# Performance work log

Measured on AMD Instinct MI355X. Metric: run time of the kernel, lower is better.

The kernel has to match this reference:

```python
import jax, jax.numpy as jnp
import numpy as np

B, T, C, H = 4, 8192, 1024, 8
D = C // H  # head dim = 128

def setup_inputs() -> dict:
    key = jax.random.key(0)
    ks = jax.random.split(key, 9)
    s = 1.0 / np.sqrt(C)
    return {
        "x":  jax.random.normal(ks[0], (B, T, C), dtype=jnp.float32),
        "Wq": jax.random.normal(ks[1], (C, C), dtype=jnp.float32) * s,
        "bq": jax.random.normal(ks[2], (C,), dtype=jnp.float32) * s,
        "Wk": jax.random.normal(ks[3], (C, C), dtype=jnp.float32) * s,
        "bk": jax.random.normal(ks[4], (C,), dtype=jnp.float32) * s,
        "Wv": jax.random.normal(ks[5], (C, C), dtype=jnp.float32) * s,
        "bv": jax.random.normal(ks[6], (C,), dtype=jnp.float32) * s,
        "Wp": jax.random.normal(ks[7], (C, C), dtype=jnp.float32) * s,
        "bp": jax.random.normal(ks[8], (C,), dtype=jnp.float32) * s,
    }

def _heads(t):
    # [B, T, C] -> [B, H, T, D]
    return t.reshape(B, T, H, D).transpose(0, 2, 1, 3)

def reference(x, Wq, bq, Wk, bk, Wv, bv, Wp, bp):
    q = _heads(x @ Wq + bq)  # [B,H,T,D]
    k = _heads(x @ Wk + bk)
    v = _heads(x @ Wv + bv)
    # attn_type == 'l1': softmax over head/feature dim
    q = jax.nn.softmax(q, axis=-1)
    k = jax.nn.softmax(k, axis=-1)
    k_sum = k.sum(axis=-2, keepdims=True)                      # [B,H,1,D]
    D_inv = 1.0 / (q * k_sum).sum(axis=-1, keepdims=True)      # [B,H,T,1]
    context = jnp.einsum('bhtd,bhte->bhde', k, v)              # [B,H,D,D]
    y = jnp.einsum('bhtd,bhde->bhte', q, context) * D_inv + q  # [B,H,T,D]
    y = y.transpose(0, 2, 1, 3).reshape(B, T, C)               # merge heads
    return y @ Wp + bp
```

## Files before the change

kernel.cpp:

```cpp
#include <hip/hip_runtime.h>

#define B_ 4
#define T_ 8192
#define C_ 1024
#define H_ 8
#define D_ 128
#define M_ (B_*T_)
#define NKC_ 32

typedef __attribute__((ext_vector_type(8))) short bf16x8;
typedef __attribute__((ext_vector_type(4))) float f32x4;

__device__ __forceinline__ unsigned short f2b(float f) {
  union { float f; unsigned int u; } x; x.f = f;
  unsigned int r = x.u + 0x7fffu + ((x.u >> 16) & 1u);
  return (unsigned short)(r >> 16);
}
__device__ __forceinline__ float b2f(unsigned short u) {
  union { float f; unsigned int u; } x; x.u = ((unsigned int)u) << 16; return x.f;
}

__device__ __forceinline__ void gl2lds16(const void* g, void* l) {
  __builtin_amdgcn_global_load_lds((const __attribute__((address_space(1))) void*)g,
                                   (__attribute__((address_space(3))) void*)l, 16, 0, 0);
}

__device__ __forceinline__ int swz_id() {
  const int orig = blockIdx.y * 8 + blockIdx.x;
  return (orig & 7) * 256 + (orig >> 3);
}

template<typename OutT, bool VTRANS=false>
__global__ __launch_bounds__(256) void mfma_gemm_bias(
    const unsigned short* __restrict__ A,
    const unsigned short* __restrict__ Bt,
    const float* __restrict__ bias,
    OutT* __restrict__ out,
    int M, int N, int K)
{
  __shared__ __align__(16) char lds[32768];
  char* As = lds;
  char* Bs = lds + 16384;
  const int tid  = threadIdx.x;
  const int w    = tid >> 6, lane = tid & 63;
  const int id   = swz_id();
  const int bm   = (id >> 3) * 128, bn = (id & 7) * 128;
  const int wrow = (w >> 1) * 64, wcol = (w & 1) * 64;
  const int l15  = lane & 15, l4 = lane >> 4;

  f32x4 acc[4][4] = {};

  const int srow = lane >> 3;
  const int sc   = lane & 7;

  for (int k0 = 0; k0 < K; k0 += 64) {
    __syncthreads();
#pragma unroll
    for (int j = 0; j < 4; ++j) {
      const int ch  = w * 4 + j;
      const int row = ch * 8 + srow;
      const int kc  = sc ^ (row & 7);
      const char* ga = (const char*)(A  + (size_t)(bm + row) * K + k0) + kc * 16;
      const char* gb = (const char*)(Bt + (size_t)(bn + row) * K + k0) + kc * 16;
      gl2lds16(ga, As + ch * 1024 + lane * 16);
      gl2lds16(gb, Bs + ch * 1024 + lane * 16);
    }
    __syncthreads();

#pragma unroll
    for (int ks = 0; ks < 2; ++ks) {
      bf16x8 af[4], bf[4];
#pragma unroll
      for (int i = 0; i < 4; ++i) {
        const int m  = wrow + i * 16 + l15;
        const int n  = wcol + i * 16 + l15;
        const int kc = ks * 4 + l4;
        af[i] = *(const bf16x8*)(As + m * 128 + ((kc ^ (m & 7)) * 16));
        bf[i] = *(const bf16x8*)(Bs + n * 128 + ((kc ^ (n & 7)) * 16));
      }
#pragma unroll
      for (int i = 0; i < 4; ++i)
#pragma unroll
        for (int j = 0; j < 4; ++j)
          acc[i][j] = __builtin_amdgcn_mfma_f32_16x16x32_bf16(af[i], bf[j], acc[i][j], 0, 0, 0);
    }
  }

#pragma unroll
  for (int j = 0; j < 4; ++j) {
    const int col = bn + wcol + j * 16 + l15;
    const float bv = bias[col];
    if constexpr (VTRANS) {
      const int e = wcol + j * 16 + l15;
      const int h = bn >> 7;
#pragma unroll
      for (int i = 0; i < 4; ++i) {
        const int m = bm + wrow + i * 16 + l4 * 4;
        const int b = m >> 13, t = m & 8191;
        union { unsigned short u[4]; uint2 v; } pk;
#pragma unroll
        for (int r = 0; r < 4; ++r) pk.u[r] = f2b(acc[i][j][r] + bv);
        *(uint2*)((unsigned short*)out + ((size_t)(b * H_ + h) * D_ + e) * T_ + t) = pk.v;
      }
    } else {
#pragma unroll
      for (int i = 0; i < 4; ++i) {
        const int rbase = bm + wrow + i * 16 + l4 * 4;
#pragma unroll
        for (int r = 0; r < 4; ++r) {
          const float val = acc[i][j][r] + bv;
          if constexpr (sizeof(OutT) == 4)
            out[(size_t)(rbase + r) * N + col] = val;
          else
            ((unsigned short*)out)[(size_t)(rbase + r) * N + col] = f2b(val);
        }
      }
    }
  }
}

template<bool KMODE>
__global__ __launch_bounds__(256) void qk_gemm_softmax(
    const unsigned short* __restrict__ A,
    const unsigned short* __restrict__ Bt,
    const float* __restrict__ bias,
    unsigned short* __restrict__ kT,
    unsigned short* __restrict__ qb,
    float* __restrict__ ksum,
    const float* __restrict__ ksum_in,
    float* __restrict__ dinv)
{
  __shared__ __align__(16) char lds[32768];
  char* As = lds;
  char* Bs = lds + 16384;
  const int tid  = threadIdx.x;
  const int w    = tid >> 6, lane = tid & 63;
  const int id   = swz_id();
  const int bm   = (id >> 3) * 128, bn = (id & 7) * 128;
  const int wrow = w * 32;
  const int l15  = lane & 15, l4 = lane >> 4;

  f32x4 acc[2][8] = {};
  const int srow = lane >> 3;
  const int sc   = lane & 7;

  for (int k0 = 0; k0 < 1024; k0 += 64) {
    __syncthreads();
#pragma unroll
    for (int j = 0; j < 4; ++j) {
      const int ch  = w * 4 + j;
      const int row = ch * 8 + srow;
      const int kc  = sc ^ (row & 7);
      gl2lds16((const char*)(A  + (size_t)(bm + row) * 1024 + k0) + kc * 16, As + ch * 1024 + lane * 16);
      gl2lds16((const char*)(Bt + (size_t)(bn + row) * 1024 + k0) + kc * 16, Bs + ch * 1024 + lane * 16);
    }
    __syncthreads();

#pragma unroll
    for (int ks = 0; ks < 2; ++ks) {
      bf16x8 af[2], bf[8];
      const int kc = ks * 4 + l4;
#pragma unroll
      for (int i = 0; i < 2; ++i) {
        const int m = wrow + i * 16 + l15;
        af[i] = *(const bf16x8*)(As + m * 128 + ((kc ^ (m & 7)) * 16));
      }
#pragma unroll
      for (int j = 0; j < 8; ++j) {
        const int n = j * 16 + l15;
        bf[j] = *(const bf16x8*)(Bs + n * 128 + ((kc ^ (n & 7)) * 16));
      }
#pragma unroll
      for (int i = 0; i < 2; ++i)
#pragma unroll
        for (int j = 0; j < 8; ++j)
          acc[i][j] = __builtin_amdgcn_mfma_f32_16x16x32_bf16(af[i], bf[j], acc[i][j], 0, 0, 0);
    }
  }

  float bvj[8];
#pragma unroll
  for (int j = 0; j < 8; ++j) bvj[j] = bias[bn + j * 16 + l15];

#pragma unroll
  for (int i = 0; i < 2; ++i)
#pragma unroll
    for (int r = 0; r < 4; ++r) {
      float v[8];
      float mx = -1e30f;
#pragma unroll
      for (int j = 0; j < 8; ++j) { v[j] = acc[i][j][r] + bvj[j]; mx = fmaxf(mx, v[j]); }
#pragma unroll
      for (int off = 8; off > 0; off >>= 1) mx = fmaxf(mx, __shfl_xor(mx, off, 64));
      float s = 0.f;
#pragma unroll
      for (int j = 0; j < 8; ++j) { v[j] = expf(v[j] - mx); s += v[j]; }
#pragma unroll
      for (int off = 8; off > 0; off >>= 1) s += __shfl_xor(s, off, 64);
      const float inv = 1.0f / s;
#pragma unroll
      for (int j = 0; j < 8; ++j) acc[i][j][r] = v[j] * inv;
    }

  const int h  = bn >> 7;
  const int b  = bm >> 13;
  const int bh = b * 8 + h;

  if constexpr (KMODE) {
    float csum[8];
#pragma unroll
    for (int j = 0; j < 8; ++j) csum[j] = 0.f;
#pragma unroll
    for (int j = 0; j < 8; ++j) {
      const int d = j * 16 + l15;
#pragma unroll
      for (int i = 0; i < 2; ++i) {
        const int t = (bm + wrow + i * 16 + l4 * 4) & 8191;
        union { unsigned short u[4]; uint2 v2; } pk;
#pragma unroll
        for (int r = 0; r < 4; ++r) {
          const unsigned short us = f2b(acc[i][j][r]);
          pk.u[r] = us;
          csum[j] += b2f(us);
        }
        *(uint2*)(kT + ((size_t)bh * 128 + d) * 8192 + t) = pk.v2;
      }
    }
#pragma unroll
    for (int j = 0; j < 8; ++j) {
      csum[j] += __shfl_xor(csum[j], 16, 64);
      csum[j] += __shfl_xor(csum[j], 32, 64);
    }
    __syncthreads();
    float* red = (float*)lds;
    if (l4 == 0) {
#pragma unroll
      for (int j = 0; j < 8; ++j) red[w * 128 + j * 16 + l15] = csum[j];
    }
    __syncthreads();
    if (tid < 128) {
      const float s2 = red[tid] + red[128 + tid] + red[256 + tid] + red[384 + tid];
      atomicAdd(&ksum[(size_t)bh * 128 + tid], s2);
    }
  } else {
    float ks8[8];
#pragma unroll
    for (int j = 0; j < 8; ++j) ks8[j] = ksum_in[(size_t)bh * 128 + j * 16 + l15];
#pragma unroll
    for (int i = 0; i < 2; ++i)
#pragma unroll
      for (int r = 0; r < 4; ++r) {
        const int m = bm + wrow + i * 16 + l4 * 4 + r;
        float dot = 0.f;
#pragma unroll
        for (int j = 0; j < 8; ++j) {
          acc[i][j][r] = b2f(f2b(acc[i][j][r]));
          dot += acc[i][j][r] * ks8[j];
        }
#pragma unroll
        for (int off = 8; off > 0; off >>= 1) dot += __shfl_xor(dot, off, 64);
        if (l15 == 0) dinv[(size_t)bh * 8192 + (m & 8191)] = 1.0f / dot;
#pragma unroll
        for (int j = 0; j < 8; ++j)
          qb[(size_t)m * 1024 + bn + j * 16 + l15] = f2b(acc[i][j][r]);
      }
  }
}

__global__ __launch_bounds__(256) void ctx_part_mfma(
    const unsigned short* __restrict__ kT,
    const unsigned short* __restrict__ vT,
    float* __restrict__ part)
{
  __shared__ __align__(16) char lds[32768];
  char* As = lds;
  char* Bs = lds + 16384;
  const int tid  = threadIdx.x;
  const int w    = tid >> 6, lane = tid & 63;
  const int bh   = blockIdx.y;
  const int kbase = blockIdx.x * (T_ / NKC_);
  const int wrow = (w >> 1) * 64, wcol = (w & 1) * 64;
  const int l15  = lane & 15, l4 = lane >> 4;
  const unsigned short* A  = kT + (size_t)bh * (D_ * T_);
  const unsigned short* Bt = vT + (size_t)bh * (D_ * T_);

  f32x4 acc[4][4] = {};
  const int srow = lane >> 3;
  const int sc   = lane & 7;

  for (int k0 = kbase; k0 < kbase + (T_ / NKC_); k0 += 64) {
    __syncthreads();
#pragma unroll
    for (int j = 0; j < 4; ++j) {
      const int ch  = w * 4 + j;
      const int row = ch * 8 + srow;
      const int kc  = sc ^ (row & 7);
      gl2lds16((const char*)(A  + (size_t)row * T_ + k0) + kc * 16, As + ch * 1024 + lane * 16);
      gl2lds16((const char*)(Bt + (size_t)row * T_ + k0) + kc * 16, Bs + ch * 1024 + lane * 16);
    }
    __syncthreads();

#pragma unroll
    for (int ks = 0; ks < 2; ++ks) {
      bf16x8 af[4], bf[4];
#pragma unroll
      for (int i = 0; i < 4; ++i) {
        const int m  = wrow + i * 16 + l15;
        const int n  = wcol + i * 16 + l15;
        const int kc = ks * 4 + l4;
        af[i] = *(const bf16x8*)(As + m * 128 + ((kc ^ (m & 7)) * 16));
        bf[i] = *(const bf16x8*)(Bs + n * 128 + ((kc ^ (n & 7)) * 16));
      }
#pragma unroll
      for (int i = 0; i < 4; ++i)
#pragma unroll
        for (int j = 0; j < 4; ++j)
          acc[i][j] = __builtin_amdgcn_mfma_f32_16x16x32_bf16(af[i], bf[j], acc[i][j], 0, 0, 0);
    }
  }

  float* cb = part + ((size_t)blockIdx.x * 32 + bh) * (D_ * D_);
#pragma unroll
  for (int j = 0; j < 4; ++j) {
    const int e = wcol + j * 16 + l15;
#pragma unroll
    for (int i = 0; i < 4; ++i) {
      const int dbase = wrow + i * 16 + l4 * 4;
      *(f32x4*)&cb[(size_t)e * D_ + dbase] = acc[i][j];
    }
  }
}

__global__ __launch_bounds__(256) void ctx_reduce(
    const float* __restrict__ part, unsigned short* __restrict__ ctxTb)
{
  const size_t i = ((size_t)blockIdx.x * 256 + threadIdx.x) * 4;
  float4 a = {0.f, 0.f, 0.f, 0.f};
#pragma unroll 4
  for (int p = 0; p < NKC_; ++p) {
    float4 v = *(const float4*)(part + (size_t)p * (32 * D_ * D_) + i);
    a.x += v.x; a.y += v.y; a.z += v.z; a.w += v.w;
  }
  union { unsigned short u[4]; uint2 v2; } pk;
  pk.u[0] = f2b(a.x); pk.u[1] = f2b(a.y); pk.u[2] = f2b(a.z); pk.u[3] = f2b(a.w);
  *(uint2*)(ctxTb + i) = pk.v2;
}

__global__ __launch_bounds__(256) void y_mfma(
    const unsigned short* __restrict__ qb,
    const unsigned short* __restrict__ ctxTb,
    const float* __restrict__ dinv,
    unsigned short* __restrict__ yb)
{
  __shared__ __align__(16) char lds[32768];
  char* As = lds;
  char* Bs = lds + 16384;
  const int tid  = threadIdx.x;
  const int w    = tid >> 6, lane = tid & 63;
  const int id   = swz_id();
  const int bm   = (id >> 3) * 128, bn = (id & 7) * 128;
  const int wrow = (w >> 1) * 64, wcol = (w & 1) * 64;
  const int l15  = lane & 15, l4 = lane >> 4;
  const int h = bn >> 7, b = bm >> 13, bh = b * 8 + h;
  const unsigned short* Bt = ctxTb + (size_t)bh * (D_ * D_);

  f32x4 acc[4][4] = {};
  const int srow = lane >> 3;
  const int sc   = lane & 7;

#pragma unroll
  for (int k0 = 0; k0 < 128; k0 += 64) {
    __syncthreads();
#pragma unroll
    for (int j = 0; j < 4; ++j) {
      const int ch  = w * 4 + j;
      const int row = ch * 8 + srow;
      const int kc  = sc ^ (row & 7);
      gl2lds16((const char*)(qb + (size_t)(bm + row) * 1024 + bn + k0) + kc * 16, As + ch * 1024 + lane * 16);
      gl2lds16((const char*)(Bt + (size_t)row * 128 + k0) + kc * 16, Bs + ch * 1024 + lane * 16);
    }
    __syncthreads();

#pragma unroll
    for (int ks = 0; ks < 2; ++ks) {
      bf16x8 af[4], bf[4];
#pragma unroll
      for (int i = 0; i < 4; ++i) {
        const int m  = wrow + i * 16 + l15;
        const int n  = wcol + i * 16 + l15;
        const int kc = ks * 4 + l4;
        af[i] = *(const bf16x8*)(As + m * 128 + ((kc ^ (m & 7)) * 16));
        bf[i] = *(const bf16x8*)(Bs + n * 128 + ((kc ^ (n & 7)) * 16));
      }
#pragma unroll
      for (int i = 0; i < 4; ++i)
#pragma unroll
        for (int j = 0; j < 4; ++j)
          acc[i][j] = __builtin_amdgcn_mfma_f32_16x16x32_bf16(af[i], bf[j], acc[i][j], 0, 0, 0);
    }
  }

  float di[4][4];
#pragma unroll
  for (int i = 0; i < 4; ++i)
#pragma unroll
    for (int r = 0; r < 4; ++r)
      di[i][r] = dinv[(size_t)bh * 8192 + ((bm + wrow + i * 16 + l4 * 4 + r) & 8191)];

#pragma unroll
  for (int j = 0; j < 4; ++j) {
    const int col = bn + wcol + j * 16 + l15;
#pragma unroll
    for (int i = 0; i < 4; ++i) {
      const int m = bm + wrow + i * 16 + l4 * 4;
#pragma unroll
      for (int r = 0; r < 4; ++r) {
        const float qv = b2f(qb[(size_t)(m + r) * 1024 + col]);
        yb[(size_t)(m + r) * 1024 + col] = f2b(fmaf(acc[i][j][r], di[i][r], qv));
      }
    }
  }
}

__global__ __launch_bounds__(256) void conv_bf16(
    const float* __restrict__ in, unsigned short* __restrict__ out)
{
  const size_t i = ((size_t)blockIdx.x * 256 + threadIdx.x) * 8;
  float4 a = *(const float4*)(in + i);
  float4 b = *(const float4*)(in + i + 4);
  union { unsigned short s[8]; uint4 v; } pk;
  pk.s[0] = f2b(a.x); pk.s[1] = f2b(a.y); pk.s[2] = f2b(a.z); pk.s[3] = f2b(a.w);
  pk.s[4] = f2b(b.x); pk.s[5] = f2b(b.y); pk.s[6] = f2b(b.z); pk.s[7] = f2b(b.w);
  *(uint4*)(out + i) = pk.v;
}

__global__ __launch_bounds__(256) void convT_w(
    const float* __restrict__ W, unsigned short* __restrict__ Wt)
{
  __shared__ float s[32][33];
  const int k0 = blockIdx.x * 32, n0 = blockIdx.y * 32;
  const int tx = threadIdx.x & 31, ty = threadIdx.x >> 5;
#pragma unroll
  for (int r = ty; r < 32; r += 8) s[r][tx] = W[(size_t)(k0 + r) * 1024 + n0 + tx];
  __syncthreads();
#pragma unroll
  for (int r = ty; r < 32; r += 8) Wt[(size_t)(n0 + r) * 1024 + k0 + tx] = f2b(s[tx][r]);
}

extern "C" void kernel_launch(void* const* d_in, const int* in_sizes, int n_in,
                              void* d_out, int out_size, void* d_ws, size_t ws_size,
                              hipStream_t stream)
{
  const float* x  = (const float*)d_in[0];
  const float* Wq = (const float*)d_in[1];
  const float* bq = (const float*)d_in[2];
  const float* Wk = (const float*)d_in[3];
  const float* bk = (const float*)d_in[4];
  const float* Wv = (const float*)d_in[5];
  const float* bv = (const float*)d_in[6];
  const float* Wp = (const float*)d_in[7];
  const float* bp = (const float*)d_in[8];
  float* out = (float*)d_out;

  char* w = (char*)d_ws;
  unsigned short* xb  = (unsigned short*)w;
  unsigned short* qb  = (unsigned short*)(w + (64UL  << 20));
  unsigned short* kT  = (unsigned short*)(w + (128UL << 20));
  unsigned short* vT  = (unsigned short*)(w + (192UL << 20));
  unsigned short* Wtq = (unsigned short*)(w + (256UL << 20));
  unsigned short* Wtk = Wtq + 1024*1024;
  unsigned short* Wtv = Wtk + 1024*1024;
  unsigned short* Wtp = Wtv + 1024*1024;
  float* ksum  = (float*)(w + (264UL << 20));
  float* dinv  = (float*)(w + (265UL << 20));
  unsigned short* ctxTb = (unsigned short*)(w + (266UL << 20));
  float* part  = (float*)(w + (268UL << 20));
  unsigned short* yb = xb;

  hipMemsetAsync(ksum, 0, 16384, stream);

  dim3 blk(256);
  dim3 gconvT(32, 32);
  dim3 ggemm(C_/128, M_/128);

  conv_bf16<<<dim3(M_*C_/2048), blk, 0, stream>>>(x, xb);
  convT_w<<<gconvT, blk, 0, stream>>>(Wq, Wtq);
  convT_w<<<gconvT, blk, 0, stream>>>(Wk, Wtk);
  convT_w<<<gconvT, blk, 0, stream>>>(Wv, Wtv);
  convT_w<<<gconvT, blk, 0, stream>>>(Wp, Wtp);

  qk_gemm_softmax<true><<<ggemm, blk, 0, stream>>>(xb, Wtk, bk, kT, nullptr, ksum, nullptr, nullptr);
  mfma_gemm_bias<unsigned short, true><<<ggemm, blk, 0, stream>>>(xb, Wtv, bv, vT, M_, C_, C_);
  qk_gemm_softmax<false><<<ggemm, blk, 0, stream>>>(xb, Wtq, bq, nullptr, qb, nullptr, ksum, dinv);

  ctx_part_mfma<<<dim3(NKC_, B_*H_), blk, 0, stream>>>(kT, vT, part);
  ctx_reduce   <<<dim3(32*D_*D_/1024), blk, 0, stream>>>(part, ctxTb);
  y_mfma<<<ggemm, blk, 0, stream>>>(qb, ctxTb, dinv, yb);

  mfma_gemm_bias<float><<<ggemm, blk, 0, stream>>>(yb, Wtp, bp, out, M_, C_, C_);
}
```

Measured before the change: 767.4 us.

## Double-buffer LDS staging in all MFMA GEMM kernels and merge weight transposes

Each MFMA GEMM kernel (projection GEMM, qk softmax GEMM, context partial, y GEMM) now keeps two LDS buffers. It issues the global-to-LDS loads for the next K tile before computing on the current one, with one barrier per iteration instead of two. The aim is to hide global load latency behind MFMA work. The cost is doubling LDS per block to 64KB, which may lower occupancy. The four weight transpose launches are also merged into one launch with a z grid dimension.

Result: faster. 708.5 us (-7.7%).

```diff
diff --git a/kernel.cpp b/kernel.cpp
--- a/kernel.cpp
+++ b/kernel.cpp
@@ -38,35 +38,36 @@
     OutT* __restrict__ out,
     int M, int N, int K)
 {
-  __shared__ __align__(16) char lds[32768];
-  char* As = lds;
-  char* Bs = lds + 16384;
+  __shared__ __align__(16) char lds[65536];
   const int tid  = threadIdx.x;
   const int w    = tid >> 6, lane = tid & 63;
   const int id   = swz_id();
   const int bm   = (id >> 3) * 128, bn = (id & 7) * 128;
   const int wrow = (w >> 1) * 64, wcol = (w & 1) * 64;
   const int l15  = lane & 15, l4 = lane >> 4;
-
-  f32x4 acc[4][4] = {};
-
-  const int srow = lane >> 3;
-  const int sc   = lane & 7;
-
-  for (int k0 = 0; k0 < K; k0 += 64) {
-    __syncthreads();
+  const int srow = lane >> 3, sc = lane & 7;
+
+  auto stage = [&](int buf, int k0) {
+    char* As = lds + buf * 32768;
+    char* Bs = As + 16384;
 #pragma unroll
     for (int j = 0; j < 4; ++j) {
       const int ch  = w * 4 + j;
       const int row = ch * 8 + srow;
       const int kc  = sc ^ (row & 7);
-      const char* ga = (const char*)(A  + (size_t)(bm + row) * K + k0) + kc * 16;
-      const char* gb = (const char*)(Bt + (size_t)(bn + row) * K + k0) + kc * 16;
-      gl2lds16(ga, As + ch * 1024 + lane * 16);
-      gl2lds16(gb, Bs + ch * 1024 + lane * 16);
-    }
-    __syncthreads();
-
+      gl2lds16((const char*)(A  + (size_t)(bm + row) * K + k0) + kc * 16, As + ch * 1024 + lane * 16);
+      gl2lds16((const char*)(Bt + (size_t)(bn + row) * K + k0) + kc * 16, Bs + ch * 1024 + lane * 16);
+    }
+  };
+
+  f32x4 acc[4][4] = {};
+  stage(0, 0);
+  __syncthreads();
+  int cur = 0;
+  for (int k0 = 0; k0 < K; k0 += 64) {
+    if (k0 + 64 < K) stage(cur ^ 1, k0 + 64);
+    const char* As = lds + cur * 32768;
+    const char* Bs = As + 16384;
 #pragma unroll
     for (int ks = 0; ks < 2; ++ks) {
       bf16x8 af[4], bf[4];
@@ -84,6 +85,8 @@
         for (int j = 0; j < 4; ++j)
           acc[i][j] = __builtin_amdgcn_mfma_f32_16x16x32_bf16(af[i], bf[j], acc[i][j], 0, 0, 0);
     }
+    __syncthreads();
+    cur ^= 1;
   }
 
 #pragma unroll
@@ -130,22 +133,18 @@
     const float* __restrict__ ksum_in,
     float* __restrict__ dinv)
 {
-  __shared__ __align__(16) char lds[32768];
-  char* As = lds;
-  char* Bs = lds + 16384;
+  __shared__ __align__(16) char lds[65536];
   const int tid  = threadIdx.x;
   const int w    = tid >> 6, lane = tid & 63;
   const int id   = swz_id();
   const int bm   = (id >> 3) * 128, bn = (id & 7) * 128;
   const int wrow = w * 32;
   const int l15  = lane & 15, l4 = lane >> 4;
-
-  f32x4 acc[2][8] = {};
-  const int srow = lane >> 3;
-  const int sc   = lane & 7;
-
-  for (int k0 = 0; k0 < 1024; k0 += 64) {
-    __syncthreads();
+  const int srow = lane >> 3, sc = lane & 7;
+
+  auto stage = [&](int buf, int k0) {
+    char* As = lds + buf * 32768;
+    char* Bs = As + 16384;
 #pragma unroll
     for (int j = 0; j < 4; ++j) {
       const int ch  = w * 4 + j;
@@ -154,8 +153,16 @@
       gl2lds16((const char*)(A  + (size_t)(bm + row) * 1024 + k0) + kc * 16, As + ch * 1024 + lane * 16);
       gl2lds16((const char*)(Bt + (size_t)(bn + row) * 1024 + k0) + kc * 16, Bs + ch * 1024 + lane * 16);
     }
-    __syncthreads();
-
+  };
+
+  f32x4 acc[2][8] = {};
+  stage(0, 0);
+  __syncthreads();
+  int cur = 0;
+  for (int k0 = 0; k0 < 1024; k0 += 64) {
+    if (k0 + 64 < 1024) stage(cur ^ 1, k0 + 64);
+    const char* As = lds + cur * 32768;
+    const char* Bs = As + 16384;
 #pragma unroll
     for (int ks = 0; ks < 2; ++ks) {
       bf16x8 af[2], bf[8];
@@ -176,6 +183,8 @@
         for (int j = 0; j < 8; ++j)
           acc[i][j] = __builtin_amdgcn_mfma_f32_16x16x32_bf16(af[i], bf[j], acc[i][j], 0, 0, 0);
     }
+    __syncthreads();
+    cur ^= 1;
   }
 
   float bvj[8];
@@ -272,24 +281,20 @@
     const unsigned short* __restrict__ vT,
     float* __restrict__ part)
 {
-  __shared__ __align__(16) char lds[32768];
-  char* As = lds;
-  char* Bs = lds + 16384;
+  __shared__ __align__(16) char lds[65536];
   const int tid  = threadIdx.x;
   const int w    = tid >> 6, lane = tid & 63;
   const int bh   = blockIdx.y;
   const int kbase = blockIdx.x * (T_ / NKC_);
   const int wrow = (w >> 1) * 64, wcol = (w & 1) * 64;
   const int l15  = lane & 15, l4 = lane >> 4;
+  const int srow = lane >> 3, sc = lane & 7;
   const unsigned short* A  = kT + (size_t)bh * (D_ * T_);
   const unsigned short* Bt = vT + (size_t)bh * (D_ * T_);
 
-  f32x4 acc[4][4] = {};
-  const int srow = lane >> 3;
-  const int sc   = lane & 7;
-
-  for (int k0 = kbase; k0 < kbase + (T_ / NKC_); k0 += 64) {
-    __syncthreads();
+  auto stage = [&](int buf, int k0) {
+    char* As = lds + buf * 32768;
+    char* Bs = As + 16384;
 #pragma unroll
     for (int j = 0; j < 4; ++j) {
       const int ch  = w * 4 + j;
@@ -298,8 +303,16 @@
       gl2lds16((const char*)(A  + (size_t)row * T_ + k0) + kc * 16, As + ch * 1024 + lane * 16);
       gl2lds16((const char*)(Bt + (size_t)row * T_ + k0) + kc * 16, Bs + ch * 1024 + lane * 16);
     }
-    __syncthreads();
-
+  };
+
+  f32x4 acc[4][4] = {};
+  stage(0, kbase);
+  __syncthreads();
+  int cur = 0;
+  for (int k0 = kbase; k0 < kbase + (T_ / NKC_); k0 += 64) {
+    if (k0 + 64 < kbase + (T_ / NKC_)) stage(cur ^ 1, k0 + 64);
+    const char* As = lds + cur * 32768;
+    const char* Bs = As + 16384;
 #pragma unroll
     for (int ks = 0; ks < 2; ++ks) {
       bf16x8 af[4], bf[4];
@@ -317,6 +330,8 @@
         for (int j = 0; j < 4; ++j)
           acc[i][j] = __builtin_amdgcn_mfma_f32_16x16x32_bf16(af[i], bf[j], acc[i][j], 0, 0, 0);
     }
+    __syncthreads();
+    cur ^= 1;
   }
 
   float* cb = part + ((size_t)blockIdx.x * 32 + bh) * (D_ * D_);
@@ -352,25 +367,20 @@
     const float* __restrict__ dinv,
     unsigned short* __restrict__ yb)
 {
-  __shared__ __align__(16) char lds[32768];
-  char* As = lds;
-  char* Bs = lds + 16384;
+  __shared__ __align__(16) char lds[65536];
   const int tid  = threadIdx.x;
   const int w    = tid >> 6, lane = tid & 63;
   const int id   = swz_id();
   const int bm   = (id >> 3) * 128, bn = (id & 7) * 128;
   const int wrow = (w >> 1) * 64, wcol = (w & 1) * 64;
   const int l15  = lane & 15, l4 = lane >> 4;
+  const int srow = lane >> 3, sc = lane & 7;
   const int h = bn >> 7, b = bm >> 13, bh = b * 8 + h;
   const unsigned short* Bt = ctxTb + (size_t)bh * (D_ * D_);
 
-  f32x4 acc[4][4] = {};
-  const int srow = lane >> 3;
-  const int sc   = lane & 7;
-
-#pragma unroll
-  for (int k0 = 0; k0 < 128; k0 += 64) {
-    __syncthreads();
+  auto stage = [&](int buf, int k0) {
+    char* As = lds + buf * 32768;
+    char* Bs = As + 16384;
 #pragma unroll
     for (int j = 0; j < 4; ++j) {
       const int ch  = w * 4 + j;
@@ -379,8 +389,17 @@
       gl2lds16((const char*)(qb + (size_t)(bm + row) * 1024 + bn + k0) + kc * 16, As + ch * 1024 + lane * 16);
       gl2lds16((const char*)(Bt + (size_t)row * 128 + k0) + kc * 16, Bs + ch * 1024 + lane * 16);
     }
-    __syncthreads();
-
+  };
+
+  f32x4 acc[4][4] = {};
+  stage(0, 0);
+  __syncthreads();
+  int cur = 0;
+#pragma unroll
+  for (int k0 = 0; k0 < 128; k0 += 64) {
+    if (k0 + 64 < 128) stage(cur ^ 1, k0 + 64);
+    const char* As = lds + cur * 32768;
+    const char* Bs = As + 16384;
 #pragma unroll
     for (int ks = 0; ks < 2; ++ks) {
       bf16x8 af[4], bf[4];
@@ -398,6 +417,8 @@
         for (int j = 0; j < 4; ++j)
           acc[i][j] = __builtin_amdgcn_mfma_f32_16x16x32_bf16(af[i], bf[j], acc[i][j], 0, 0, 0);
     }
+    __syncthreads();
+    cur ^= 1;
   }
 
   float di[4][4];
@@ -434,9 +455,14 @@
   *(uint4*)(out + i) = pk.v;
 }
 
-__global__ __launch_bounds__(256) void convT_w(
-    const float* __restrict__ W, unsigned short* __restrict__ Wt)
-{
+__global__ __launch_bounds__(256) void convT_w4(
+    const float* __restrict__ W0, const float* __restrict__ W1,
+    const float* __restrict__ W2, const float* __restrict__ W3,
+    unsigned short* __restrict__ Wt0)
+{
+  const int z = blockIdx.z;
+  const float* W = (z == 0) ? W0 : (z == 1) ? W1 : (z == 2) ? W2 : W3;
+  unsigned short* Wt = Wt0 + (size_t)z * 1024 * 1024;
   __shared__ float s[32][33];
   const int k0 = blockIdx.x * 32, n0 = blockIdx.y * 32;
   const int tx = threadIdx.x & 31, ty = threadIdx.x >> 5;
@@ -480,14 +506,10 @@
   hipMemsetAsync(ksum, 0, 16384, stream);
 
   dim3 blk(256);
-  dim3 gconvT(32, 32);
   dim3 ggemm(C_/128, M_/128);
 
   conv_bf16<<<dim3(M_*C_/2048), blk, 0, stream>>>(x, xb);
-  convT_w<<<gconvT, blk, 0, stream>>>(Wq, Wtq);
-  convT_w<<<gconvT, blk, 0, stream>>>(Wk, Wtk);
-  convT_w<<<gconvT, blk, 0, stream>>>(Wv, Wtv);
-  convT_w<<<gconvT, blk, 0, stream>>>(Wp, Wtp);
+  convT_w4<<<dim3(32, 32, 4), blk, 0, stream>>>(Wq, Wk, Wv, Wp, Wtq);
 
   qk_gemm_softmax<true><<<ggemm, blk, 0, stream>>>(xb, Wtk, bk, kT, nullptr, ksum, nullptr, nullptr);
   mfma_gemm_bias<unsigned short, true><<<ggemm, blk, 0, stream>>>(xb, Wtv, bv, vT, M_, C_, C_);
```
